# Performance work log

Measured on AMD Instinct MI355X. Metric: run time of the kernel, lower is better.

The kernel has to match this reference:

```python
import jax, jax.numpy as jnp
import numpy as np

EPS = 1e-6

def _l2norm(x, axis=-1):
    # F.normalize with eps=1e-12 clamp on the norm
    n = jnp.sqrt(jnp.sum(x * x, axis=axis, keepdims=True))
    return x / jnp.maximum(n, 1e-12)

def setup_inputs() -> dict:
    key = jax.random.key(0)
    k1, k2, k3, k4 = jax.random.split(key, 4)
    B, D = 512, 512
    mu1 = jax.random.normal(k1, (B, D), dtype=jnp.float32)
    mu2 = jax.random.normal(k2, (B, D), dtype=jnp.float32)
    sigma1_sq = jax.random.uniform(k3, (B, D), dtype=jnp.float32)
    sigma2_sq = jax.random.uniform(k4, (B, D), dtype=jnp.float32)
    logit_scale = jnp.float32(100.0)  # CLIP-style exp(t)
    return {"mu1": mu1, "sigma1_sq": sigma1_sq, "mu2": mu2,
            "sigma2_sq": sigma2_sq, "logit_scale": logit_scale}

def _bd_similarity(mu1, sigma1_sq, mu2, sigma2_sq):
    # Bhattacharyya-distance-based similarity matrix [B, B]
    n1 = _l2norm(mu1)
    n2 = _l2norm(mu2)
    B, D = n1.shape
    sigma_avg = 0.5 * (sigma1_sq[:, None, :] + sigma2_sq[None, :, :])  # [B,B,D]
    diff = n1[:, None, :] - n2[None, :, :]                              # [B,B,D]
    term1 = jnp.sum(diff * diff / (sigma_avg + EPS), axis=2)            # [B,B]
    log_det_avg = jnp.sum(jnp.log(sigma_avg + EPS), axis=2)             # [B,B]
    log_det1 = jnp.sum(jnp.log(sigma1_sq + EPS), axis=1)[:, None]       # [B,1]
    log_det2 = jnp.sum(jnp.log(sigma2_sq + EPS), axis=1)[None, :]       # [1,B]
    term2 = log_det_avg - 0.5 * (log_det1 + log_det2)
    bd = 0.125 * term1 + 0.5 * term2
    return jnp.exp(-bd / D)

def _confident_loss(mu1, sigma1_sq, mu2, sigma2_sq):
    n1 = _l2norm(mu1)
    n2 = _l2norm(mu2)
    B = n1.shape[0]
    # ||n1_i - n2_j||^2 via Gram expansion (no BxBxD intermediate)
    sq1 = jnp.sum(n1 * n1, axis=1)[:, None]
    sq2 = jnp.sum(n2 * n2, axis=1)[None, :]
    d2 = sq1 + sq2 - 2.0 * (n1 @ n2.T)                                  # [B,B]
    sim = jnp.exp(-d2)
    diag = jnp.diagonal(sim)                                            # [B]
    # topk k=1 over off-diagonal == row max with diagonal masked out
    neg_inf = jnp.asarray(-jnp.inf, sim.dtype)
    off = jnp.where(jnp.eye(B, dtype=bool), neg_inf, sim)
    neg_max = jnp.max(off, axis=1)                                      # [B]
    uncertainty = jnp.exp(-diag / neg_max)                              # [B]
    avg_sigma = 0.5 * (jnp.mean(sigma1_sq, axis=1) + jnp.mean(sigma2_sq, axis=1))
    var_loss = jnp.mean(uncertainty)
    u_n = _l2norm(uncertainty, axis=-1)
    s_n = _l2norm(avg_sigma, axis=-1)
    cos_sim = jnp.sum(u_n * s_n)  # both already unit vectors
    return 1.0 - cos_sim, var_loss * 0.5

def _cross_entropy_diag(logits):
    # mean CE with labels = arange(B): -log_softmax(logits)[i, i]
    return -jnp.mean(jnp.diagonal(jax.nn.log_softmax(logits, axis=1)))

def reference(mu1, sigma1_sq, mu2, sigma2_sq, logit_scale):
    sim = _bd_similarity(mu1, sigma1_sq, mu2, sigma2_sq)
    logits = logit_scale * sim
    loss_pro = 0.5 * (_cross_entropy_diag(logits) + _cross_entropy_diag(logits.T))
    loss_rank, var_loss = _confident_loss(mu1, sigma1_sq, mu2, sigma2_sq)
    return loss_pro, loss_rank * 2.4, var_loss
```

## Files before the change

kernel.cpp:

```cpp
#include <hip/hip_runtime.h>
#include <math.h>

#define BDIM 512
#define DDIM 512

constexpr float EPS   = 1e-6f;
constexpr float HEPS  = 0.5e-6f;
constexpr float LN2   = 0.6931471805599453f;
constexpr float LOG2E = 1.4426950408889634f;

__device__ __forceinline__ float wave_reduce_sum(float v) {
  #pragma unroll
  for (int o = 32; o > 0; o >>= 1) v += __shfl_down(v, o, 64);
  return v;
}
__device__ __forceinline__ float wave_reduce_max(float v) {
  #pragma unroll
  for (int o = 32; o > 0; o >>= 1) v = fmaxf(v, __shfl_down(v, o, 64));
  return v;
}

__global__ __launch_bounds__(256) void prep_kernel(
    const float* __restrict__ mu1, const float* __restrict__ s1,
    const float* __restrict__ mu2, const float* __restrict__ s2,
    float2* __restrict__ pA, float2* __restrict__ pB,
    float* __restrict__ ld,
    float* __restrict__ mrow) {
  const int r = blockIdx.x;
  const int which = blockIdx.y;
  const float* __restrict__ mu = which ? mu2 : mu1;
  const float* __restrict__ sg = which ? s2 : s1;
  float2* __restrict__ pout = which ? pB : pA;
  const int t = threadIdx.x;

  const float a  = mu[r * DDIM + t];
  const float b  = mu[r * DDIM + t + 256];
  const float sa = sg[r * DDIM + t];
  const float sb = sg[r * DDIM + t + 256];

  float v0 = a * a + b * b;
  float v1 = __log2f(sa + EPS) + __log2f(sb + EPS);
  float v2 = sa + sb;

  __shared__ float red[3][4];
  __shared__ float sinv;
  const int wid = t >> 6, lane = t & 63;
  v0 = wave_reduce_sum(v0);
  v1 = wave_reduce_sum(v1);
  v2 = wave_reduce_sum(v2);
  if (lane == 0) { red[0][wid] = v0; red[1][wid] = v1; red[2][wid] = v2; }
  __syncthreads();
  if (t == 0) {
    float sq = red[0][0] + red[0][1] + red[0][2] + red[0][3];
    float lg = red[1][0] + red[1][1] + red[1][2] + red[1][3];
    float sm = red[2][0] + red[2][1] + red[2][2] + red[2][3];
    ld[which * BDIM + r]   = LN2 * lg;
    mrow[which * BDIM + r] = sm * (1.0f / DDIM);
    sinv = 1.0f / fmaxf(sqrtf(sq), 1e-12f);
  }
  __syncthreads();
  const float inv = sinv;
  pout[r * DDIM + t]       = make_float2(a * inv, fmaf(0.5f, sa, HEPS));
  pout[r * DDIM + t + 256] = make_float2(b * inv, fmaf(0.5f, sb, HEPS));
}

#define GSTRIDE 65
#define GHALF   (32 * GSTRIDE)

__global__ __launch_bounds__(256) void bd_kernel(
    const float2* __restrict__ pA, const float2* __restrict__ pB,
    float* __restrict__ t1p, float* __restrict__ ldap,
    float* __restrict__ dacp) {
  __shared__ __align__(16) float2 tile[2 * GHALF];

  const int t  = threadIdx.x;
  const int i0 = blockIdx.y * 32, j0 = blockIdx.x * 32;
  const int z  = blockIdx.z;
  const int il = (t >> 4) * 2;
  const int jl = (t & 15) * 2;

  #pragma unroll
  for (int q = 0; q < 8; ++q) {
    const int idx = q * 256 + t;
    const int arr = idx >> 10;
    const int rem = idx & 1023;
    const int row = rem >> 5;
    const int c4  = rem & 31;
    const float2* __restrict__ src = arr ? pB : pA;
    const int grow = (arr ? j0 : i0) + row;
    const float4 v = *(const float4*)&src[grow * DDIM + z * 64 + c4 * 2];
    float2* dst = tile + arr * GHALF + row * GSTRIDE + c4 * 2;
    dst[0] = make_float2(v.x, v.y);
    dst[1] = make_float2(v.z, v.w);
  }
  __syncthreads();

  float t1[2][2]  = {{0.f,0.f},{0.f,0.f}};
  float lda[2][2] = {{0.f,0.f},{0.f,0.f}};
  float dac[2][2] = {{0.f,0.f},{0.f,0.f}};

  const float2* a0p = tile + il * GSTRIDE;
  const float2* a1p = tile + (il + 1) * GSTRIDE;
  const float2* b0p = tile + GHALF + jl * GSTRIDE;
  const float2* b1p = tile + GHALF + (jl + 1) * GSTRIDE;

  for (int g8 = 0; g8 < 8; ++g8) {
    float m[2][2] = {{1.f,1.f},{1.f,1.f}};
    #pragma unroll
    for (int k = 0; k < 8; ++k) {
      const int d = g8 * 8 + k;
      const float2 A0 = a0p[d], A1 = a1p[d];
      const float2 B0 = b0p[d], B1 = b1p[d];
      #define UPD(ii, jj, Av, Bv)                                            \
        {                                                                    \
          const float sv = Av.y + Bv.y;                                      \
          const float df = Av.x - Bv.x;                                      \
          t1[ii][jj] = fmaf(df * df, __builtin_amdgcn_rcpf(sv), t1[ii][jj]); \
          m[ii][jj] *= sv;                                                   \
          dac[ii][jj] = fmaf(Av.x, Bv.x, dac[ii][jj]);                       \
        }
      UPD(0, 0, A0, B0) UPD(0, 1, A0, B1)
      UPD(1, 0, A1, B0) UPD(1, 1, A1, B1)
      #undef UPD
    }
    lda[0][0] += __log2f(m[0][0]);
    lda[0][1] += __log2f(m[0][1]);
    lda[1][0] += __log2f(m[1][0]);
    lda[1][1] += __log2f(m[1][1]);
  }

  const size_t zb = (size_t)z * BDIM * BDIM;
  #pragma unroll
  for (int ii = 0; ii < 2; ++ii) {
    const size_t o = zb + (size_t)(i0 + il + ii) * BDIM + j0 + jl;
    *(float2*)&t1p[o]  = make_float2(t1[ii][0],  t1[ii][1]);
    *(float2*)&ldap[o] = make_float2(lda[ii][0], lda[ii][1]);
    *(float2*)&dacp[o] = make_float2(dac[ii][0], dac[ii][1]);
  }
}

__global__ __launch_bounds__(256) void combine_kernel(
    const float* __restrict__ t1p, const float* __restrict__ ldap,
    const float* __restrict__ dacp, const float* __restrict__ ld,
    const float* __restrict__ lscale,
    float* __restrict__ sim, float* __restrict__ pmaxf,
    float* __restrict__ pdiag, float* __restrict__ lse_row,
    float* __restrict__ dlog) {
  const int i = blockIdx.x;
  const int t = threadIdx.x;
  const float l1 = ld[i];
  const float sc = *lscale;
  float rmax = 0.f;
  float lg[2];
  #pragma unroll
  for (int q = 0; q < 2; ++q) {
    const int j = t + q * 256;
    const size_t o = (size_t)i * BDIM + j;
    float t1 = 0.f, lda = 0.f, dac = 0.f;
    #pragma unroll
    for (int zz = 0; zz < 8; ++zz) {
      const size_t idx = (size_t)zz * BDIM * BDIM + o;
      t1 += t1p[idx]; lda += ldap[idx]; dac += dacp[idx];
    }
    const float bd = fmaf(0.125f, t1,
                          0.5f * (LN2 * lda - 0.5f * (l1 + ld[BDIM + j])));
    const float sv = exp2f(bd * (-LOG2E / (float)DDIM));
    sim[o] = sv;
    lg[q] = sc * sv;
    const float p = exp2f((2.0f * LOG2E) * dac);
    if (j == i) { pdiag[i] = p; dlog[i] = sc * sv; }
    else        rmax = fmaxf(rmax, p);
  }
  __shared__ float red[4];
  const int wid = t >> 6, lane = t & 63;

  float wm = wave_reduce_max(rmax);
  if (lane == 0) red[wid] = wm;
  __syncthreads();
  if (t == 0) pmaxf[i] = fmaxf(fmaxf(red[0], red[1]), fmaxf(red[2], red[3]));
  __syncthreads();

  float rm = wave_reduce_max(fmaxf(lg[0], lg[1]));
  if (lane == 0) red[wid] = rm;
  __syncthreads();
  rm = fmaxf(fmaxf(red[0], red[1]), fmaxf(red[2], red[3]));
  __syncthreads();
  float rs = wave_reduce_sum(exp2f((lg[0] - rm) * LOG2E) +
                             exp2f((lg[1] - rm) * LOG2E));
  if (lane == 0) red[wid] = rs;
  __syncthreads();
  if (t == 0)
    lse_row[i] = rm + LN2 * __log2f(red[0] + red[1] + red[2] + red[3]);
}

__global__ __launch_bounds__(256) void lse_col_kernel(
    const float* __restrict__ sim, const float* __restrict__ lscale,
    float* __restrict__ lse_col) {
  const int b = blockIdx.x;
  const int t = threadIdx.x;
  const float sc = *lscale;
  const float c0 = sc * sim[t * BDIM + b];
  const float c1 = sc * sim[(t + 256) * BDIM + b];

  __shared__ float red[4];
  const int wid = t >> 6, lane = t & 63;

  float cm = wave_reduce_max(fmaxf(c0, c1));
  if (lane == 0) red[wid] = cm;
  __syncthreads();
  cm = fmaxf(fmaxf(red[0], red[1]), fmaxf(red[2], red[3]));
  __syncthreads();

  float cs = wave_reduce_sum(exp2f((c0 - cm) * LOG2E) + exp2f((c1 - cm) * LOG2E));
  if (lane == 0) red[wid] = cs;
  __syncthreads();
  if (t == 0)
    lse_col[b] = cm + LN2 * __log2f(red[0] + red[1] + red[2] + red[3]);
}

__global__ __launch_bounds__(512) void final_kernel(
    const float* __restrict__ pdiag, const float* __restrict__ pmaxf,
    const float* __restrict__ mrow, const float* __restrict__ lse_row,
    const float* __restrict__ lse_col, const float* __restrict__ dlog,
    float* __restrict__ out) {
  const int t = threadIdx.x;
  const float pm = pmaxf[t];
  const float u  = exp2f(-(pdiag[t] / pm) * LOG2E);
  const float as = 0.5f * (mrow[t] + mrow[BDIM + t]);

  float vals[6];
  vals[0] = u;
  vals[1] = u * u;
  vals[2] = as * as;
  vals[3] = u * as;
  vals[4] = lse_row[t] - dlog[t];
  vals[5] = lse_col[t] - dlog[t];

  __shared__ float red[6][8];
  const int wid = t >> 6, lane = t & 63;
  #pragma unroll
  for (int k = 0; k < 6; ++k) {
    const float v = wave_reduce_sum(vals[k]);
    if (lane == 0) red[k][wid] = v;
  }
  __syncthreads();
  if (t == 0) {
    float s[6];
    #pragma unroll
    for (int k = 0; k < 6; ++k) {
      float a = 0.f;
      #pragma unroll
      for (int w = 0; w < 8; ++w) a += red[k][w];
      s[k] = a;
    }
    const float mean_u = s[0] * (1.0f / BDIM);
    const float cosv = s[3] / fmaxf(sqrtf(s[1]) * sqrtf(s[2]), 1e-24f);
    out[0] = 0.5f * (s[4] + s[5]) * (1.0f / BDIM);
    out[1] = 2.4f * (1.0f - cosv);
    out[2] = 0.5f * mean_u;
  }
}

extern "C" void kernel_launch(void* const* d_in, const int* in_sizes, int n_in,
                              void* d_out, int out_size, void* d_ws, size_t ws_size,
                              hipStream_t stream) {
  const float* mu1 = (const float*)d_in[0];
  const float* s1  = (const float*)d_in[1];
  const float* mu2 = (const float*)d_in[2];
  const float* s2  = (const float*)d_in[3];
  const float* lsc = (const float*)d_in[4];
  float* out = (float*)d_out;

  float* ws      = (float*)d_ws;
  float2* pA     = (float2*)ws;
  float2* pB     = pA + BDIM * DDIM;
  float* sim     = (float*)(pB + BDIM * DDIM);
  float* t1p     = sim + BDIM * BDIM;
  float* ldap    = t1p + 8 * BDIM * BDIM;
  float* dacp    = ldap + 8 * BDIM * BDIM;
  float* ld      = dacp + 8 * BDIM * BDIM;
  float* mrow    = ld + 2 * BDIM;
  float* pmaxf   = mrow + 2 * BDIM;
  float* pdiag   = pmaxf + BDIM;
  float* lse_row = pdiag + BDIM;
  float* lse_col = lse_row + BDIM;
  float* dlog    = lse_col + BDIM;

  prep_kernel<<<dim3(BDIM, 2), 256, 0, stream>>>(mu1, s1, mu2, s2, pA, pB,
                                                 ld, mrow);
  bd_kernel<<<dim3(16, 16, 8), 256, 0, stream>>>(pA, pB, t1p, ldap, dacp);
  combine_kernel<<<BDIM, 256, 0, stream>>>(t1p, ldap, dacp, ld, lsc, sim,
                                           pmaxf, pdiag, lse_row, dlog);
  lse_col_kernel<<<BDIM, 256, 0, stream>>>(sim, lsc, lse_col);
  final_kernel<<<1, 512, 0, stream>>>(pdiag, pmaxf, mrow, lse_row, lse_col,
                                      dlog, out);
}
```

Measured before the change: 56.02 us.

## Enlarge BD tile to 64x64 with 4x4 register blocking and split planar layout

The pairwise Bhattacharyya kernel now computes a 64x64 output tile per block, with each thread holding a 4x4 strided micro-tile instead of 2x2. The prep kernel writes normalized mu and half-sigma as separate planar arrays so they can be staged as float4 vectors into padded LDS. The aim is to cut LDS reads per FLOP and global reloads of the inputs by raising register reuse. The cost is more registers per thread, which can lower occupancy, and only 512 blocks in the grid instead of 2048.

```diff
diff --git a/kernel.cpp b/kernel.cpp
--- a/kernel.cpp
+++ b/kernel.cpp
@@ -23,14 +23,16 @@
 __global__ __launch_bounds__(256) void prep_kernel(
     const float* __restrict__ mu1, const float* __restrict__ s1,
     const float* __restrict__ mu2, const float* __restrict__ s2,
-    float2* __restrict__ pA, float2* __restrict__ pB,
+    float* __restrict__ nA, float* __restrict__ sA,
+    float* __restrict__ nB, float* __restrict__ sB,
     float* __restrict__ ld,
     float* __restrict__ mrow) {
   const int r = blockIdx.x;
   const int which = blockIdx.y;
   const float* __restrict__ mu = which ? mu2 : mu1;
   const float* __restrict__ sg = which ? s2 : s1;
-  float2* __restrict__ pout = which ? pB : pA;
+  float* __restrict__ nout = which ? nB : nA;
+  float* __restrict__ sout = which ? sB : sA;
   const int t = threadIdx.x;
 
   const float a  = mu[r * DDIM + t];
@@ -60,82 +62,100 @@
   }
   __syncthreads();
   const float inv = sinv;
-  pout[r * DDIM + t]       = make_float2(a * inv, fmaf(0.5f, sa, HEPS));
-  pout[r * DDIM + t + 256] = make_float2(b * inv, fmaf(0.5f, sb, HEPS));
-}
-
-#define GSTRIDE 65
-#define GHALF   (32 * GSTRIDE)
+  nout[r * DDIM + t]       = a * inv;
+  nout[r * DDIM + t + 256] = b * inv;
+  sout[r * DDIM + t]       = fmaf(0.5f, sa, HEPS);
+  sout[r * DDIM + t + 256] = fmaf(0.5f, sb, HEPS);
+}
 
 __global__ __launch_bounds__(256) void bd_kernel(
-    const float2* __restrict__ pA, const float2* __restrict__ pB,
+    const float* __restrict__ nA, const float* __restrict__ sA,
+    const float* __restrict__ nB, const float* __restrict__ sB,
     float* __restrict__ t1p, float* __restrict__ ldap,
     float* __restrict__ dacp) {
-  __shared__ __align__(16) float2 tile[2 * GHALF];
+  __shared__ __align__(16) float4 lds[4 * 64 * 17];
 
   const int t  = threadIdx.x;
-  const int i0 = blockIdx.y * 32, j0 = blockIdx.x * 32;
+  const int i0 = blockIdx.y * 64, j0 = blockIdx.x * 64;
   const int z  = blockIdx.z;
-  const int il = (t >> 4) * 2;
-  const int jl = (t & 15) * 2;
-
-  #pragma unroll
-  for (int q = 0; q < 8; ++q) {
-    const int idx = q * 256 + t;
-    const int arr = idx >> 10;
-    const int rem = idx & 1023;
-    const int row = rem >> 5;
-    const int c4  = rem & 31;
-    const float2* __restrict__ src = arr ? pB : pA;
-    const int grow = (arr ? j0 : i0) + row;
-    const float4 v = *(const float4*)&src[grow * DDIM + z * 64 + c4 * 2];
-    float2* dst = tile + arr * GHALF + row * GSTRIDE + c4 * 2;
-    dst[0] = make_float2(v.x, v.y);
-    dst[1] = make_float2(v.z, v.w);
-  }
-  __syncthreads();
-
-  float t1[2][2]  = {{0.f,0.f},{0.f,0.f}};
-  float lda[2][2] = {{0.f,0.f},{0.f,0.f}};
-  float dac[2][2] = {{0.f,0.f},{0.f,0.f}};
-
-  const float2* a0p = tile + il * GSTRIDE;
-  const float2* a1p = tile + (il + 1) * GSTRIDE;
-  const float2* b0p = tile + GHALF + jl * GSTRIDE;
-  const float2* b1p = tile + GHALF + (jl + 1) * GSTRIDE;
-
-  for (int g8 = 0; g8 < 8; ++g8) {
-    float m[2][2] = {{1.f,1.f},{1.f,1.f}};
-    #pragma unroll
-    for (int k = 0; k < 8; ++k) {
-      const int d = g8 * 8 + k;
-      const float2 A0 = a0p[d], A1 = a1p[d];
-      const float2 B0 = b0p[d], B1 = b1p[d];
-      #define UPD(ii, jj, Av, Bv)                                            \
-        {                                                                    \
-          const float sv = Av.y + Bv.y;                                      \
-          const float df = Av.x - Bv.x;                                      \
-          t1[ii][jj] = fmaf(df * df, __builtin_amdgcn_rcpf(sv), t1[ii][jj]); \
-          m[ii][jj] *= sv;                                                   \
-          dac[ii][jj] = fmaf(Av.x, Bv.x, dac[ii][jj]);                       \
+  const int ti = t >> 4;
+  const int tj = t & 15;
+
+  {
+    const float* __restrict__ srcs[4] = { nA, sA, nB, sB };
+    #pragma unroll
+    for (int it = 0; it < 16; ++it) {
+      const int arr = it >> 2;
+      const int rem = (it & 3) * 256 + t;
+      const int row = rem >> 4;
+      const int dc  = rem & 15;
+      const int grow = (arr < 2 ? i0 : j0) + row;
+      lds[arr * 1088 + row * 17 + dc] =
+          *(const float4*)&srcs[arr][grow * DDIM + z * 64 + dc * 4];
+    }
+  }
+  __syncthreads();
+
+  float t1[4][4]  = {};
+  float lda[4][4] = {};
+  float dac[4][4] = {};
+
+  const float4* __restrict__ pAn = lds + 0 * 1088 + ti * 17;
+  const float4* __restrict__ pAs = lds + 1 * 1088 + ti * 17;
+  const float4* __restrict__ pBn = lds + 2 * 1088 + tj * 17;
+  const float4* __restrict__ pBs = lds + 3 * 1088 + tj * 17;
+
+  for (int g2 = 0; g2 < 8; ++g2) {
+    float m[4][4] = {{1.f,1.f,1.f,1.f},{1.f,1.f,1.f,1.f},
+                     {1.f,1.f,1.f,1.f},{1.f,1.f,1.f,1.f}};
+    #pragma unroll
+    for (int h = 0; h < 2; ++h) {
+      const int dc = g2 * 2 + h;
+      float4 An[4], As[4], Bn[4], Bs[4];
+      #pragma unroll
+      for (int q = 0; q < 4; ++q) {
+        An[q] = pAn[q * 272 + dc];
+        As[q] = pAs[q * 272 + dc];
+        Bn[q] = pBn[q * 272 + dc];
+        Bs[q] = pBs[q * 272 + dc];
+      }
+      #pragma unroll
+      for (int dd = 0; dd < 4; ++dd) {
+        #pragma unroll
+        for (int qi = 0; qi < 4; ++qi) {
+          const float an = ((const float*)&An[qi])[dd];
+          const float as = ((const float*)&As[qi])[dd];
+          #pragma unroll
+          for (int qj = 0; qj < 4; ++qj) {
+            const float bn = ((const float*)&Bn[qj])[dd];
+            const float bs = ((const float*)&Bs[qj])[dd];
+            const float sv = as + bs;
+            const float df = an - bn;
+            t1[qi][qj]  = fmaf(df * df, __builtin_amdgcn_rcpf(sv), t1[qi][qj]);
+            m[qi][qj]  *= sv;
+            dac[qi][qj] = fmaf(an, bn, dac[qi][qj]);
+          }
         }
-      UPD(0, 0, A0, B0) UPD(0, 1, A0, B1)
-      UPD(1, 0, A1, B0) UPD(1, 1, A1, B1)
-      #undef UPD
-    }
-    lda[0][0] += __log2f(m[0][0]);
-    lda[0][1] += __log2f(m[0][1]);
-    lda[1][0] += __log2f(m[1][0]);
-    lda[1][1] += __log2f(m[1][1]);
+      }
+    }
+    #pragma unroll
+    for (int qi = 0; qi < 4; ++qi)
+      #pragma unroll
+      for (int qj = 0; qj < 4; ++qj)
+        lda[qi][qj] += __log2f(m[qi][qj]);
   }
 
   const size_t zb = (size_t)z * BDIM * BDIM;
   #pragma unroll
-  for (int ii = 0; ii < 2; ++ii) {
-    const size_t o = zb + (size_t)(i0 + il + ii) * BDIM + j0 + jl;
-    *(float2*)&t1p[o]  = make_float2(t1[ii][0],  t1[ii][1]);
-    *(float2*)&ldap[o] = make_float2(lda[ii][0], lda[ii][1]);
-    *(float2*)&dacp[o] = make_float2(dac[ii][0], dac[ii][1]);
+  for (int qi = 0; qi < 4; ++qi) {
+    #pragma unroll
+    for (int qj = 0; qj < 4; ++qj) {
+      const size_t o = zb + (size_t)(i0 + 16 * qi + ti) * BDIM
+                          + j0 + 16 * qj + tj;
+      t1p[o]  = t1[qi][qj];
+      ldap[o] = lda[qi][qj];
+      dacp[o] = dac[qi][qj];
+    }
   }
 }
 
@@ -272,9 +292,11 @@
   float* out = (float*)d_out;
 
   float* ws      = (float*)d_ws;
-  float2* pA     = (float2*)ws;
-  float2* pB     = pA + BDIM * DDIM;
-  float* sim     = (float*)(pB + BDIM * DDIM);
+  float* nA      = ws;
+  float* sA      = nA + BDIM * DDIM;
+  float* nB      = sA + BDIM * DDIM;
+  float* sB      = nB + BDIM * DDIM;
+  float* sim     = sB + BDIM * DDIM;
   float* t1p     = sim + BDIM * BDIM;
   float* ldap    = t1p + 8 * BDIM * BDIM;
   float* dacp    = ldap + 8 * BDIM * BDIM;
@@ -286,9 +308,10 @@
   float* lse_col = lse_row + BDIM;
   float* dlog    = lse_col + BDIM;
 
-  prep_kernel<<<dim3(BDIM, 2), 256, 0, stream>>>(mu1, s1, mu2, s2, pA, pB,
-                                                 ld, mrow);
-  bd_kernel<<<dim3(16, 16, 8), 256, 0, stream>>>(pA, pB, t1p, ldap, dacp);
+  prep_kernel<<<dim3(BDIM, 2), 256, 0, stream>>>(mu1, s1, mu2, s2, nA, sA,
+                                                 nB, sB, ld, mrow);
+  bd_kernel<<<dim3(8, 8, 8), 256, 0, stream>>>(nA, sA, nB, sB, t1p, ldap,
+                                               dacp);
   combine_kernel<<<BDIM, 256, 0, stream>>>(t1p, ldap, dacp, ld, lsc, sim,
                                            pmaxf, pdiag, lse_row, dlog);
   lse_col_kernel<<<BDIM, 256, 0, stream>>>(sim, lsc, lse_col);
```

New measurement: 58.72 us. 1.05x slower.
